# Performance work log

Hardware: AMD Instinct MI355X
Metric: run time of the kernel (lower is better)

## Reference

```python
import jax, jax.numpy as jnp
import numpy as np

N, E, IN, H, C = 20000, 320000, 512, 4, 64
HC = H * C
EPS_BN = 1e-5


def setup_inputs() -> dict:
    key = jax.random.key(0)
    ks = jax.random.split(key, 12)
    p = lambda k, shape, s=0.05: jax.random.normal(k, shape, dtype=jnp.float32) * s
    z = lambda n: jnp.zeros((n,), jnp.float32)
    o = lambda n: jnp.ones((n,), jnp.float32)
    return {
        "x": jax.random.normal(ks[0], (N, IN), dtype=jnp.float32),
        "edge_index": jax.random.randint(ks[1], (2, E), 0, N),
        "Wl0": p(ks[2], (IN, HC)), "Wr0": p(ks[3], (IN, HC)),
        "att0": p(ks[4], (H, C)), "b0": z(HC),
        "g0": o(HC), "be0": z(HC), "m0": z(HC), "v0": o(HC),
        "Wl1": p(ks[5], (HC, HC)), "Wr1": p(ks[6], (HC, HC)),
        "att1": p(ks[7], (H, C)), "b1": z(HC),
        "g1": o(HC), "be1": z(HC), "m1": z(HC), "v1": o(HC),
        "Wl2": p(ks[8], (HC, 2)), "Wr2": p(ks[9], (HC, 2)),
        "att2": p(ks[10], (1, 2)), "b2": z(2),
    }


def gatv2_conv(x, Wl, Wr, att, b, ei, concat):
    # GATv2: e_ij = att . LeakyReLU(Wl x_j + Wr x_i); softmax over in-edges of i
    n = x.shape[0]
    h, c = att.shape
    xl = (x @ Wl).reshape(n, h, c)  # source/message transform
    xr = (x @ Wr).reshape(n, h, c)  # target transform
    src, dst = ei[0], ei[1]
    m = xl[src] + xr[dst]                                   # [E,H,C] edge gather
    e = jnp.sum(jax.nn.leaky_relu(m, 0.2) * att, axis=-1)   # [E,H]
    emax = jax.ops.segment_max(e, dst, num_segments=n)      # segment softmax
    emax = jnp.where(jnp.isfinite(emax), emax, 0.0)
    ex = jnp.exp(e - emax[dst])
    denom = jax.ops.segment_sum(ex, dst, num_segments=n)
    alpha = ex / (denom[dst] + 1e-16)                       # [E,H]
    out = jax.ops.segment_sum(alpha[:, :, None] * xl[src], dst, num_segments=n)
    out = out.reshape(n, h * c) if concat else out.mean(axis=1)
    return out + b


def bn_eval(x, g, be, m, v):
    return (x - m) * (g * jax.lax.rsqrt(v + EPS_BN)) + be


def reference(x, edge_index, Wl0, Wr0, att0, b0, g0, be0, m0, v0,
              Wl1, Wr1, att1, b1, g1, be1, m1, v1, Wl2, Wr2, att2, b2):
    loops = jnp.arange(N)
    ei = jnp.concatenate([edge_index, jnp.stack([loops, loops])], axis=1)
    h = gatv2_conv(x, Wl0, Wr0, att0, b0, ei, True)
    h = jax.nn.elu(bn_eval(h, g0, be0, m0, v0))
    h = gatv2_conv(h, Wl1, Wr1, att1, b1, ei, True)
    h = jax.nn.elu(bn_eval(h, g1, be1, m1, v1))
    out = gatv2_conv(h, Wl2, Wr2, att2, b2, ei, False)
    return jax.nn.log_softmax(out, axis=1)
```

## Files before the change

kernel.cpp:

```cpp
#include <hip/hip_runtime.h>
#include <math.h>

#define NN 20000
#define MP 20096
#define EE 320000
#define ET (EE + NN)
#define HC 256
#define EPS_BN 1e-5f

typedef __bf16 bf16x8 __attribute__((ext_vector_type(8)));
typedef float f32x4 __attribute__((ext_vector_type(4)));

__device__ __forceinline__ float4 ld4(const float* p) { return *reinterpret_cast<const float4*>(p); }
__device__ __forceinline__ float lrelu(float x) { return fmaxf(x, 0.f) + 0.2f * fminf(x, 0.f); }

__device__ __forceinline__ unsigned short f2b(float f) {
  unsigned int u = __float_as_uint(f);
  u = (u + 0x7fffu + ((u >> 16) & 1u)) >> 16;
  return (unsigned short)u;
}
__device__ __forceinline__ float b2f(unsigned short u) {
  return __uint_as_float(((unsigned int)u) << 16);
}

__device__ __forceinline__ void gld_lds16(const void* g, void* l) {
  __builtin_amdgcn_global_load_lds(
      (const __attribute__((address_space(1))) unsigned int*)g,
      (__attribute__((address_space(3))) unsigned int*)(unsigned int)(unsigned long long)l,
      16, 0, 0);
}

__global__ __launch_bounds__(256) void convert_x_kernel(const float* __restrict__ x,
                                                        unsigned short* __restrict__ xb) {
  int i = (blockIdx.x * 256 + threadIdx.x) * 4;
  if (i >= NN * 512) return;
  float4 v = ld4(&x[i]);
  ushort4 o;
  o.x = f2b(v.x); o.y = f2b(v.y); o.z = f2b(v.z); o.w = f2b(v.w);
  *reinterpret_cast<ushort4*>(&xb[i]) = o;
}

__global__ __launch_bounds__(256) void convert_w_kernel(const float* __restrict__ Wl,
                                                        const float* __restrict__ Wr,
                                                        unsigned short* __restrict__ Wf,
                                                        int K) {
  int idx = blockIdx.x * 256 + threadIdx.x;
  if (idx >= 512 * K) return;
  int n = idx / K, k = idx - n * K;
  float v = (n < 256) ? Wl[(size_t)k * 256 + n] : Wr[(size_t)k * 256 + (n - 256)];
  Wf[idx] = f2b(v);
}

__global__ __launch_bounds__(256) void gemm_mfma(const unsigned short* __restrict__ A,
                                                 const unsigned short* __restrict__ Bt,
                                                 unsigned short* __restrict__ xlb,
                                                 float* __restrict__ xrf,
                                                 int M, int K) {
  __shared__ unsigned short As[4][128 * 32];
  __shared__ unsigned short Bs[4][128 * 32];
  const int wave = threadIdx.x >> 6;
  const int lane = threadIdx.x & 63;
  const int am = lane & 15;
  const int aq = lane >> 4;
  const int wr = (wave >> 1) * 64;
  const int wc = (wave & 1) * 64;
  const int row0 = blockIdx.y * 128;
  const int col0 = blockIdx.x * 128;

  const int seg0 = wave * 128 + lane;
  const int r0 = seg0 >> 2, k0 = (seg0 & 3) * 8;
  const int seg1 = seg0 + 64;
  const int r1 = seg1 >> 2, k1 = (seg1 & 3) * 8;
  const size_t aoff0 = (size_t)(row0 + r0) * K + k0;
  const size_t aoff1 = (size_t)(row0 + r1) * K + k1;
  const size_t boff0 = (size_t)(col0 + r0) * K + k0;
  const size_t boff1 = (size_t)(col0 + r1) * K + k1;

  const int nk = K >> 5;

#define STAGE(tt, bb)                                                      \
  do {                                                                     \
    gld_lds16(A + aoff0 + (size_t)(tt) * 32, &As[bb][(wave * 128) * 8]);   \
    gld_lds16(Bt + boff0 + (size_t)(tt) * 32, &Bs[bb][(wave * 128) * 8]);  \
    gld_lds16(A + aoff1 + (size_t)(tt) * 32, &As[bb][(wave * 128 + 64) * 8]); \
    gld_lds16(Bt + boff1 + (size_t)(tt) * 32, &Bs[bb][(wave * 128 + 64) * 8]); \
  } while (0)

  f32x4 acc[4][4] = {};

  STAGE(0, 0);
  STAGE(1, 1);

  for (int t = 0; t < nk; ++t) {
    const int cur = t & 3;
    if (t + 2 < nk) {
      STAGE(t + 2, (t + 2) & 3);
      asm volatile("s_waitcnt vmcnt(8)" ::: "memory");
    } else if (t + 1 < nk) {
      asm volatile("s_waitcnt vmcnt(4)" ::: "memory");
    } else {
      asm volatile("s_waitcnt vmcnt(0)" ::: "memory");
    }
    __builtin_amdgcn_s_barrier();
    __builtin_amdgcn_sched_barrier(0);

    bf16x8 af[4], bfr[4];
#pragma unroll
    for (int i = 0; i < 4; ++i)
      af[i] = *reinterpret_cast<const bf16x8*>(&As[cur][(wr + i * 16 + am) * 32 + aq * 8]);
#pragma unroll
    for (int j = 0; j < 4; ++j)
      bfr[j] = *reinterpret_cast<const bf16x8*>(&Bs[cur][(wc + j * 16 + am) * 32 + aq * 8]);
#pragma unroll
    for (int i = 0; i < 4; ++i)
#pragma unroll
      for (int j = 0; j < 4; ++j)
        acc[i][j] = __builtin_amdgcn_mfma_f32_16x16x32_bf16(af[i], bfr[j], acc[i][j], 0, 0, 0);
  }
#undef STAGE

#pragma unroll
  for (int i = 0; i < 4; ++i) {
#pragma unroll
    for (int j = 0; j < 4; ++j) {
      int gcol = col0 + wc + j * 16 + am;
#pragma unroll
      for (int rr = 0; rr < 4; ++rr) {
        int grow = row0 + wr + i * 16 + aq * 4 + rr;
        if (grow < M) {
          float v = acc[i][j][rr];
          if (gcol < 256) xlb[(size_t)grow * 256 + gcol] = f2b(v);
          else            xrf[(size_t)grow * 256 + (gcol - 256)] = v;
        }
      }
    }
  }
}

__global__ __launch_bounds__(256) void hist_kernel(const int* __restrict__ ei,
                                                   int* __restrict__ counts) {
  int e = blockIdx.x * blockDim.x + threadIdx.x;
  if (e >= ET) return;
  int d = (e < EE) ? ei[EE + e] : (e - EE);
  atomicAdd(&counts[d], 1);
}

__global__ __launch_bounds__(1024) void scan_kernel(int* __restrict__ cursor,
                                                    int* __restrict__ offsets) {
  __shared__ int wsum[16];
  const int tid = threadIdx.x;
  const int lane = tid & 63, wv = tid >> 6;
  const int base = tid * 20;
  int vals[20];
  int s = 0;
  if (tid < 1000) {
#pragma unroll
    for (int j = 0; j < 20; ++j) { vals[j] = cursor[base + j]; s += vals[j]; }
  }
  int ssum = s;
#pragma unroll
  for (int off = 1; off < 64; off <<= 1) {
    int t = __shfl_up(ssum, off);
    if (lane >= off) ssum += t;
  }
  if (lane == 63) wsum[wv] = ssum;
  __syncthreads();
  if (wv == 0) {
    int w = (lane < 16) ? wsum[lane] : 0;
#pragma unroll
    for (int off = 1; off < 16; off <<= 1) {
      int t = __shfl_up(w, off);
      if (lane >= off) w += t;
    }
    if (lane < 16) wsum[lane] = w;
  }
  __syncthreads();
  int excl = ssum - s + (wv > 0 ? wsum[wv - 1] : 0);
  if (tid < 1000) {
    int run = excl;
#pragma unroll
    for (int j = 0; j < 20; ++j) { offsets[base + j] = run; cursor[base + j] = run; run += vals[j]; }
  }
  if (tid == 1023) offsets[NN] = wsum[15];
}

__global__ __launch_bounds__(256) void scatter_kernel(const int* __restrict__ ei,
                                                      int* __restrict__ cursor,
                                                      int* __restrict__ srcs) {
  int e = blockIdx.x * blockDim.x + threadIdx.x;
  if (e >= ET) return;
  int s, d;
  if (e < EE) { s = ei[e]; d = ei[EE + e]; } else { s = d = e - EE; }
  int pos = atomicAdd(&cursor[d], 1);
  srcs[pos] = s;
}

__global__ __launch_bounds__(256) void gat_layer(const unsigned short* __restrict__ xlb,
                                                 const float* __restrict__ xrf,
                                                 const float* __restrict__ att,
                                                 const float* __restrict__ bias,
                                                 const float* __restrict__ gam,
                                                 const float* __restrict__ bet,
                                                 const float* __restrict__ mean,
                                                 const float* __restrict__ var,
                                                 const int* __restrict__ offsets,
                                                 const int* __restrict__ srcs,
                                                 unsigned short* __restrict__ hb) {
  const int wave = threadIdx.x >> 6;
  const int lane = threadIdx.x & 63;
  const int node = blockIdx.x * 4 + wave;
  if (node >= NN) return;

  const float4 xr4 = ld4(&xrf[(size_t)node * HC + lane * 4]);
  const float4 a4 = ld4(&att[lane * 4]);
  const int beg = offsets[node];
  const int end = offsets[node + 1];

  float lA = 0.f, lB = 0.f;
  float4 OA = make_float4(0.f, 0.f, 0.f, 0.f);
  float4 OB = make_float4(0.f, 0.f, 0.f, 0.f);

  int i = beg;
  for (; i + 3 < end; i += 4) {
    int s0 = srcs[i], s1 = srcs[i + 1], s2 = srcs[i + 2], s3 = srcs[i + 3];
    ushort4 u0 = *reinterpret_cast<const ushort4*>(&xlb[(size_t)s0 * HC + lane * 4]);
    ushort4 u1 = *reinterpret_cast<const ushort4*>(&xlb[(size_t)s1 * HC + lane * 4]);
    ushort4 u2 = *reinterpret_cast<const ushort4*>(&xlb[(size_t)s2 * HC + lane * 4]);
    ushort4 u3 = *reinterpret_cast<const ushort4*>(&xlb[(size_t)s3 * HC + lane * 4]);
    float4 x0 = make_float4(b2f(u0.x), b2f(u0.y), b2f(u0.z), b2f(u0.w));
    float4 x1 = make_float4(b2f(u1.x), b2f(u1.y), b2f(u1.z), b2f(u1.w));
    float4 x2 = make_float4(b2f(u2.x), b2f(u2.y), b2f(u2.z), b2f(u2.w));
    float4 x3 = make_float4(b2f(u3.x), b2f(u3.y), b2f(u3.z), b2f(u3.w));
    float e0 = lrelu(x0.x + xr4.x) * a4.x + lrelu(x0.y + xr4.y) * a4.y +
               lrelu(x0.z + xr4.z) * a4.z + lrelu(x0.w + xr4.w) * a4.w;
    float e1 = lrelu(x1.x + xr4.x) * a4.x + lrelu(x1.y + xr4.y) * a4.y +
               lrelu(x1.z + xr4.z) * a4.z + lrelu(x1.w + xr4.w) * a4.w;
    float e2 = lrelu(x2.x + xr4.x) * a4.x + lrelu(x2.y + xr4.y) * a4.y +
               lrelu(x2.z + xr4.z) * a4.z + lrelu(x2.w + xr4.w) * a4.w;
    float e3 = lrelu(x3.x + xr4.x) * a4.x + lrelu(x3.y + xr4.y) * a4.y +
               lrelu(x3.z + xr4.z) * a4.z + lrelu(x3.w + xr4.w) * a4.w;
#pragma unroll
    for (int off = 1; off < 16; off <<= 1) {
      e0 += __shfl_xor(e0, off);
      e1 += __shfl_xor(e1, off);
      e2 += __shfl_xor(e2, off);
      e3 += __shfl_xor(e3, off);
    }
    float p0 = __expf(e0), p1 = __expf(e1), p2 = __expf(e2), p3 = __expf(e3);
    lA += p0; lB += p1; lA += p2; lB += p3;
    OA.x += p0 * x0.x; OA.y += p0 * x0.y; OA.z += p0 * x0.z; OA.w += p0 * x0.w;
    OB.x += p1 * x1.x; OB.y += p1 * x1.y; OB.z += p1 * x1.z; OB.w += p1 * x1.w;
    OA.x += p2 * x2.x; OA.y += p2 * x2.y; OA.z += p2 * x2.z; OA.w += p2 * x2.w;
    OB.x += p3 * x3.x; OB.y += p3 * x3.y; OB.z += p3 * x3.z; OB.w += p3 * x3.w;
  }
  for (; i < end; ++i) {
    int s = srcs[i];
    ushort4 u = *reinterpret_cast<const ushort4*>(&xlb[(size_t)s * HC + lane * 4]);
    float4 x0 = make_float4(b2f(u.x), b2f(u.y), b2f(u.z), b2f(u.w));
    float e = lrelu(x0.x + xr4.x) * a4.x + lrelu(x0.y + xr4.y) * a4.y +
              lrelu(x0.z + xr4.z) * a4.z + lrelu(x0.w + xr4.w) * a4.w;
#pragma unroll
    for (int off = 1; off < 16; off <<= 1) e += __shfl_xor(e, off);
    float p = __expf(e);
    lA += p;
    OA.x += p * x0.x; OA.y += p * x0.y; OA.z += p * x0.z; OA.w += p * x0.w;
  }
  float inv = 1.f / (lA + lB);
  float4 O = make_float4(OA.x + OB.x, OA.y + OB.y, OA.z + OB.z, OA.w + OB.w);

  float4 b4 = ld4(&bias[lane * 4]);
  float4 g4 = ld4(&gam[lane * 4]);
  float4 e4 = ld4(&bet[lane * 4]);
  float4 m4 = ld4(&mean[lane * 4]);
  float4 v4 = ld4(&var[lane * 4]);
  float y0 = O.x * inv + b4.x, y1 = O.y * inv + b4.y;
  float y2 = O.z * inv + b4.z, y3 = O.w * inv + b4.w;
  float z0 = (y0 - m4.x) * (g4.x * rsqrtf(v4.x + EPS_BN)) + e4.x;
  float z1 = (y1 - m4.y) * (g4.y * rsqrtf(v4.y + EPS_BN)) + e4.y;
  float z2 = (y2 - m4.z) * (g4.z * rsqrtf(v4.z + EPS_BN)) + e4.z;
  float z3 = (y3 - m4.w) * (g4.w * rsqrtf(v4.w + EPS_BN)) + e4.w;
  ushort4 r;
  r.x = f2b(z0 > 0.f ? z0 : expm1f(z0));
  r.y = f2b(z1 > 0.f ? z1 : expm1f(z1));
  r.z = f2b(z2 > 0.f ? z2 : expm1f(z2));
  r.w = f2b(z3 > 0.f ? z3 : expm1f(z3));
  *reinterpret_cast<ushort4*>(&hb[(size_t)node * HC + lane * 4]) = r;
}

__global__ __launch_bounds__(256) void lin2_kernel(const unsigned short* __restrict__ hb,
                                                   const float* __restrict__ Wl,
                                                   const float* __restrict__ Wr,
                                                   float* __restrict__ xl2,
                                                   float* __restrict__ xr2) {
  const int wave = threadIdx.x >> 6;
  const int lane = threadIdx.x & 63;
  const int node = blockIdx.x * 4 + wave;
  if (node >= NN) return;
  ushort4 h4 = *reinterpret_cast<const ushort4*>(&hb[(size_t)node * HC + lane * 4]);
  float hv[4] = {b2f(h4.x), b2f(h4.y), b2f(h4.z), b2f(h4.w)};
  float l0 = 0.f, l1 = 0.f, r0 = 0.f, r1 = 0.f;
#pragma unroll
  for (int j = 0; j < 4; ++j) {
    int row = lane * 4 + j;
    l0 += hv[j] * Wl[row * 2 + 0];
    l1 += hv[j] * Wl[row * 2 + 1];
    r0 += hv[j] * Wr[row * 2 + 0];
    r1 += hv[j] * Wr[row * 2 + 1];
  }
#pragma unroll
  for (int off = 1; off < 64; off <<= 1) {
    l0 += __shfl_xor(l0, off);
    l1 += __shfl_xor(l1, off);
    r0 += __shfl_xor(r0, off);
    r1 += __shfl_xor(r1, off);
  }
  if (lane == 0) {
    xl2[node * 2 + 0] = l0; xl2[node * 2 + 1] = l1;
    xr2[node * 2 + 0] = r0; xr2[node * 2 + 1] = r1;
  }
}

__global__ __launch_bounds__(256) void gat2_out_kernel(const float* __restrict__ xl2,
                                                       const float* __restrict__ xr2,
                                                       const float* __restrict__ att2,
                                                       const float* __restrict__ b2,
                                                       const int* __restrict__ offsets,
                                                       const int* __restrict__ srcs,
                                                       float* __restrict__ out) {
  const int wave = threadIdx.x >> 6;
  const int lane = threadIdx.x & 63;
  const int node = blockIdx.x * 4 + wave;
  if (node >= NN) return;
  const float a0 = att2[0], a1 = att2[1];
  const float xr0 = xr2[node * 2 + 0], xr1 = xr2[node * 2 + 1];
  const int beg = offsets[node], end = offsets[node + 1];

  float l = 0.f, o0 = 0.f, o1 = 0.f;
  for (int i = beg + lane; i < end; i += 64) {
    int s = srcs[i];
    float x0 = xl2[s * 2 + 0], x1 = xl2[s * 2 + 1];
    float e = lrelu(x0 + xr0) * a0 + lrelu(x1 + xr1) * a1;
    float p = __expf(e);
    l += p;
    o0 += p * x0;
    o1 += p * x1;
  }
#pragma unroll
  for (int off = 1; off < 64; off <<= 1) {
    l += __shfl_xor(l, off);
    o0 += __shfl_xor(o0, off);
    o1 += __shfl_xor(o1, off);
  }
  if (lane == 0) {
    float inv = 1.f / l;
    float t0 = o0 * inv + b2[0];
    float t1 = o1 * inv + b2[1];
    float mx = fmaxf(t0, t1);
    float ls = mx + logf(__expf(t0 - mx) + __expf(t1 - mx));
    out[node * 2 + 0] = t0 - ls;
    out[node * 2 + 1] = t1 - ls;
  }
}

extern "C" void kernel_launch(void* const* d_in, const int* in_sizes, int n_in,
                              void* d_out, int out_size, void* d_ws, size_t ws_size,
                              hipStream_t stream) {
  const float* x    = (const float*)d_in[0];
  const int*   ei   = (const int*)d_in[1];
  const float* Wl0  = (const float*)d_in[2];
  const float* Wr0  = (const float*)d_in[3];
  const float* att0 = (const float*)d_in[4];
  const float* b0   = (const float*)d_in[5];
  const float* g0   = (const float*)d_in[6];
  const float* be0  = (const float*)d_in[7];
  const float* m0   = (const float*)d_in[8];
  const float* v0   = (const float*)d_in[9];
  const float* Wl1  = (const float*)d_in[10];
  const float* Wr1  = (const float*)d_in[11];
  const float* att1 = (const float*)d_in[12];
  const float* b1   = (const float*)d_in[13];
  const float* g1   = (const float*)d_in[14];
  const float* be1  = (const float*)d_in[15];
  const float* m1   = (const float*)d_in[16];
  const float* v1   = (const float*)d_in[17];
  const float* Wl2  = (const float*)d_in[18];
  const float* Wr2  = (const float*)d_in[19];
  const float* att2 = (const float*)d_in[20];
  const float* b2   = (const float*)d_in[21];

  float* xrf = (float*)d_ws;
  unsigned short* xlb = (unsigned short*)(xrf + (size_t)NN * 256);
  unsigned short* hb  = xlb + (size_t)NN * 256;
  unsigned short* xb  = hb + (size_t)MP * 256;
  unsigned short* Wf0 = xb + (size_t)MP * 512;
  unsigned short* Wf1 = Wf0 + 512 * 512;
  float* xl2 = (float*)(Wf1 + 512 * 256);
  float* xr2 = xl2 + 2 * NN;
  int* offsets = (int*)(xr2 + 2 * NN);
  int* cursor  = offsets + (NN + 1);
  int* srcs    = cursor + NN;

  hipMemsetAsync(cursor, 0, NN * sizeof(int), stream);
  hist_kernel<<<(ET + 255) / 256, 256, 0, stream>>>(ei, cursor);
  convert_x_kernel<<<(NN * 512 / 4 + 255) / 256, 256, 0, stream>>>(x, xb);
  convert_w_kernel<<<(512 * 512 + 255) / 256, 256, 0, stream>>>(Wl0, Wr0, Wf0, 512);
  convert_w_kernel<<<(512 * 256 + 255) / 256, 256, 0, stream>>>(Wl1, Wr1, Wf1, 256);
  scan_kernel<<<1, 1024, 0, stream>>>(cursor, offsets);
  scatter_kernel<<<(ET + 255) / 256, 256, 0, stream>>>(ei, cursor, srcs);

  dim3 gemm_grid(4, MP / 128);
  gemm_mfma<<<gemm_grid, 256, 0, stream>>>(xb, Wf0, xlb, xrf, NN, 512);
  gat_layer<<<NN / 4, 256, 0, stream>>>(xlb, xrf, att0, b0, g0, be0, m0, v0, offsets, srcs, hb);
  gemm_mfma<<<gemm_grid, 256, 0, stream>>>(hb, Wf1, xlb, xrf, NN, 256);
  gat_layer<<<NN / 4, 256, 0, stream>>>(xlb, xrf, att1, b1, g1, be1, m1, v1, offsets, srcs, hb);
  lin2_kernel<<<NN / 4, 256, 0, stream>>>(hb, Wl2, Wr2, xl2, xr2);
  gat2_out_kernel<<<NN / 4, 256, 0, stream>>>(xl2, xr2, att2, b2, offsets, srcs, (float*)d_out);
}
```

Baseline: 308.8 us.

## Fuse prep kernels into one launch and use 8-wave GEMM blocks

The histogram, x conversion and both weight conversion kernels are merged into a single prep kernel that dispatches on block index, removing three launches. The MFMA GEMM now runs 512 threads (8 waves) per 128x128 tile, each wave computing a 64x32 sub-tile with one global-to-LDS load per operand per stage. The aim is more waves per tile for latency hiding and less launch overhead, at the cost of more A-fragment LDS reads per MFMA.

New measurement: 286.2 us. -7.3%, faster.

```diff
diff --git a/kernel.cpp b/kernel.cpp
--- a/kernel.cpp
+++ b/kernel.cpp
@@ -30,63 +30,79 @@
       16, 0, 0);
 }
 
-__global__ __launch_bounds__(256) void convert_x_kernel(const float* __restrict__ x,
-                                                        unsigned short* __restrict__ xb) {
-  int i = (blockIdx.x * 256 + threadIdx.x) * 4;
-  if (i >= NN * 512) return;
-  float4 v = ld4(&x[i]);
-  ushort4 o;
-  o.x = f2b(v.x); o.y = f2b(v.y); o.z = f2b(v.z); o.w = f2b(v.w);
-  *reinterpret_cast<ushort4*>(&xb[i]) = o;
-}
-
-__global__ __launch_bounds__(256) void convert_w_kernel(const float* __restrict__ Wl,
-                                                        const float* __restrict__ Wr,
-                                                        unsigned short* __restrict__ Wf,
-                                                        int K) {
-  int idx = blockIdx.x * 256 + threadIdx.x;
-  if (idx >= 512 * K) return;
+#define CXB 10000
+#define HB  ((ET + 255) / 256)
+#define W0B 1024
+#define W1B 512
+
+__device__ __forceinline__ void conv_w_body(int idx, int K, const float* Wl, const float* Wr,
+                                            unsigned short* Wf) {
   int n = idx / K, k = idx - n * K;
   float v = (n < 256) ? Wl[(size_t)k * 256 + n] : Wr[(size_t)k * 256 + (n - 256)];
   Wf[idx] = f2b(v);
 }
 
-__global__ __launch_bounds__(256) void gemm_mfma(const unsigned short* __restrict__ A,
+__global__ __launch_bounds__(256) void prep_kernel(const float* __restrict__ x,
+                                                   unsigned short* __restrict__ xb,
+                                                   const int* __restrict__ ei,
+                                                   int* __restrict__ counts,
+                                                   const float* __restrict__ Wl0,
+                                                   const float* __restrict__ Wr0,
+                                                   unsigned short* __restrict__ Wf0,
+                                                   const float* __restrict__ Wl1,
+                                                   const float* __restrict__ Wr1,
+                                                   unsigned short* __restrict__ Wf1) {
+  const int b = blockIdx.x;
+  if (b < CXB) {
+    int i = (b * 256 + threadIdx.x) * 4;
+    float4 v = ld4(&x[i]);
+    ushort4 o;
+    o.x = f2b(v.x); o.y = f2b(v.y); o.z = f2b(v.z); o.w = f2b(v.w);
+    *reinterpret_cast<ushort4*>(&xb[i]) = o;
+  } else if (b < CXB + HB) {
+    int e = (b - CXB) * 256 + threadIdx.x;
+    if (e < ET) {
+      int d = (e < EE) ? ei[EE + e] : (e - EE);
+      atomicAdd(&counts[d], 1);
+    }
+  } else if (b < CXB + HB + W0B) {
+    conv_w_body((b - CXB - HB) * 256 + threadIdx.x, 512, Wl0, Wr0, Wf0);
+  } else {
+    conv_w_body((b - CXB - HB - W0B) * 256 + threadIdx.x, 256, Wl1, Wr1, Wf1);
+  }
+}
+
+__global__ __launch_bounds__(512) void gemm_mfma(const unsigned short* __restrict__ A,
                                                  const unsigned short* __restrict__ Bt,
                                                  unsigned short* __restrict__ xlb,
                                                  float* __restrict__ xrf,
                                                  int M, int K) {
   __shared__ unsigned short As[4][128 * 32];
   __shared__ unsigned short Bs[4][128 * 32];
-  const int wave = threadIdx.x >> 6;
-  const int lane = threadIdx.x & 63;
+  const int tid = threadIdx.x;
+  const int wave = tid >> 6;
+  const int lane = tid & 63;
   const int am = lane & 15;
   const int aq = lane >> 4;
-  const int wr = (wave >> 1) * 64;
-  const int wc = (wave & 1) * 64;
+  const int wr = (wave >> 2) * 64;
+  const int wc = (wave & 3) * 32;
   const int row0 = blockIdx.y * 128;
   const int col0 = blockIdx.x * 128;
 
-  const int seg0 = wave * 128 + lane;
-  const int r0 = seg0 >> 2, k0 = (seg0 & 3) * 8;
-  const int seg1 = seg0 + 64;
-  const int r1 = seg1 >> 2, k1 = (seg1 & 3) * 8;
-  const size_t aoff0 = (size_t)(row0 + r0) * K + k0;
-  const size_t aoff1 = (size_t)(row0 + r1) * K + k1;
-  const size_t boff0 = (size_t)(col0 + r0) * K + k0;
-  const size_t boff1 = (size_t)(col0 + r1) * K + k1;
+  const int r = tid >> 2;
+  const int ks = (tid & 3) * 8;
+  const size_t aoff = (size_t)(row0 + r) * K + ks;
+  const size_t boff = (size_t)(col0 + r) * K + ks;
 
   const int nk = K >> 5;
 
-#define STAGE(tt, bb)                                                      \
-  do {                                                                     \
-    gld_lds16(A + aoff0 + (size_t)(tt) * 32, &As[bb][(wave * 128) * 8]);   \
-    gld_lds16(Bt + boff0 + (size_t)(tt) * 32, &Bs[bb][(wave * 128) * 8]);  \
-    gld_lds16(A + aoff1 + (size_t)(tt) * 32, &As[bb][(wave * 128 + 64) * 8]); \
-    gld_lds16(Bt + boff1 + (size_t)(tt) * 32, &Bs[bb][(wave * 128 + 64) * 8]); \
+#define STAGE(tt, bb)                                                    \
+  do {                                                                   \
+    gld_lds16(A + aoff + (size_t)(tt) * 32, &As[bb][wave * 512]);        \
+    gld_lds16(Bt + boff + (size_t)(tt) * 32, &Bs[bb][wave * 512]);       \
   } while (0)
 
-  f32x4 acc[4][4] = {};
+  f32x4 acc[4][2] = {};
 
   STAGE(0, 0);
   STAGE(1, 1);
@@ -95,26 +111,26 @@
     const int cur = t & 3;
     if (t + 2 < nk) {
       STAGE(t + 2, (t + 2) & 3);
-      asm volatile("s_waitcnt vmcnt(8)" ::: "memory");
+      asm volatile("s_waitcnt vmcnt(4)" ::: "memory");
     } else if (t + 1 < nk) {
-      asm volatile("s_waitcnt vmcnt(4)" ::: "memory");
+      asm volatile("s_waitcnt vmcnt(2)" ::: "memory");
     } else {
       asm volatile("s_waitcnt vmcnt(0)" ::: "memory");
     }
     __builtin_amdgcn_s_barrier();
     __builtin_amdgcn_sched_barrier(0);
 
-    bf16x8 af[4], bfr[4];
+    bf16x8 af[4], bfr[2];
 #pragma unroll
     for (int i = 0; i < 4; ++i)
       af[i] = *reinterpret_cast<const bf16x8*>(&As[cur][(wr + i * 16 + am) * 32 + aq * 8]);
 #pragma unroll
-    for (int j = 0; j < 4; ++j)
+    for (int j = 0; j < 2; ++j)
       bfr[j] = *reinterpret_cast<const bf16x8*>(&Bs[cur][(wc + j * 16 + am) * 32 + aq * 8]);
 #pragma unroll
     for (int i = 0; i < 4; ++i)
 #pragma unroll
-      for (int j = 0; j < 4; ++j)
+      for (int j = 0; j < 2; ++j)
         acc[i][j] = __builtin_amdgcn_mfma_f32_16x16x32_bf16(af[i], bfr[j], acc[i][j], 0, 0, 0);
   }
 #undef STAGE
@@ -122,7 +138,7 @@
 #pragma unroll
   for (int i = 0; i < 4; ++i) {
 #pragma unroll
-    for (int j = 0; j < 4; ++j) {
+    for (int j = 0; j < 2; ++j) {
       int gcol = col0 + wc + j * 16 + am;
 #pragma unroll
       for (int rr = 0; rr < 4; ++rr) {
@@ -135,14 +151,6 @@
       }
     }
   }
-}
-
-__global__ __launch_bounds__(256) void hist_kernel(const int* __restrict__ ei,
-                                                   int* __restrict__ counts) {
-  int e = blockIdx.x * blockDim.x + threadIdx.x;
-  if (e >= ET) return;
-  int d = (e < EE) ? ei[EE + e] : (e - EE);
-  atomicAdd(&counts[d], 1);
 }
 
 __global__ __launch_bounds__(1024) void scan_kernel(int* __restrict__ cursor,
@@ -401,17 +409,15 @@
   int* srcs    = cursor + NN;
 
   hipMemsetAsync(cursor, 0, NN * sizeof(int), stream);
-  hist_kernel<<<(ET + 255) / 256, 256, 0, stream>>>(ei, cursor);
-  convert_x_kernel<<<(NN * 512 / 4 + 255) / 256, 256, 0, stream>>>(x, xb);
-  convert_w_kernel<<<(512 * 512 + 255) / 256, 256, 0, stream>>>(Wl0, Wr0, Wf0, 512);
-  convert_w_kernel<<<(512 * 256 + 255) / 256, 256, 0, stream>>>(Wl1, Wr1, Wf1, 256);
+  prep_kernel<<<CXB + HB + W0B + W1B, 256, 0, stream>>>(x, xb, ei, cursor,
+                                                        Wl0, Wr0, Wf0, Wl1, Wr1, Wf1);
   scan_kernel<<<1, 1024, 0, stream>>>(cursor, offsets);
   scatter_kernel<<<(ET + 255) / 256, 256, 0, stream>>>(ei, cursor, srcs);
 
   dim3 gemm_grid(4, MP / 128);
-  gemm_mfma<<<gemm_grid, 256, 0, stream>>>(xb, Wf0, xlb, xrf, NN, 512);
+  gemm_mfma<<<gemm_grid, 512, 0, stream>>>(xb, Wf0, xlb, xrf, NN, 512);
   gat_layer<<<NN / 4, 256, 0, stream>>>(xlb, xrf, att0, b0, g0, be0, m0, v0, offsets, srcs, hb);
-  gemm_mfma<<<gemm_grid, 256, 0, stream>>>(hb, Wf1, xlb, xrf, NN, 256);
+  gemm_mfma<<<gemm_grid, 512, 0, stream>>>(hb, Wf1, xlb, xrf, NN, 256);
   gat_layer<<<NN / 4, 256, 0, stream>>>(xlb, xrf, att1, b1, g1, be1, m1, v1, offsets, srcs, hb);
   lin2_kernel<<<NN / 4, 256, 0, stream>>>(hb, Wl2, Wr2, xl2, xr2);
   gat2_out_kernel<<<NN / 4, 256, 0, stream>>>(xl2, xr2, att2, b2, offsets, srcs, (float*)d_out);
```
